# Performance work log

Measured on AMD Instinct MI355X. Metric: run time of the kernel, lower is better.

The kernel has to match this reference:

```python
import jax, jax.numpy as jnp
import numpy as np
import math

B, S, E, H = 2, 4096, 1024, 1024

def setup_inputs() -> dict:
    key = jax.random.key(0)
    ks = jax.random.split(key, 7)
    X = jax.random.normal(ks[0], (B, S, E), dtype=jnp.float32)
    attention_mask = jnp.ones((B, S, S), dtype=jnp.int32)
    sc = 1.0 / math.sqrt(E)
    Wq = jax.random.normal(ks[1], (H, E), dtype=jnp.float32) * sc
    Wk = jax.random.normal(ks[2], (H, E), dtype=jnp.float32) * sc
    Wv = jax.random.normal(ks[3], (H, E), dtype=jnp.float32) * sc
    bq = jnp.zeros((H,), dtype=jnp.float32)
    bk = jnp.zeros((H,), dtype=jnp.float32)
    bv = jnp.zeros((H,), dtype=jnp.float32)
    return {"X": X, "attention_mask": attention_mask,
            "Wq": Wq, "bq": bq, "Wk": Wk, "bk": bk, "Wv": Wv, "bv": bv}

def reference(X, attention_mask, Wq, bq, Wk, bk, Wv, bv):
    # Linear layers: y = x @ W^T + b (torch convention W is [out, in])
    Q = jnp.einsum('bse,he->bsh', X, Wq) + bq
    K = jnp.einsum('bse,he->bsh', X, Wk) + bk
    V = jnp.einsum('bse,he->bsh', X, Wv) + bv
    scale = 1.0 / math.sqrt(H)
    scores = jnp.einsum('bqh,bkh->bqk', Q, K) * scale  # [B,S,S]
    scores = jnp.where(attention_mask == 0, -jnp.inf, scores)
    # dropout (eval mode -> identity) would be applied here, BEFORE softmax
    weights = jax.nn.softmax(scores, axis=-1)
    out = jnp.einsum('bqk,bkh->bqh', weights, V)  # [B,S,H]
    return out
```

## Files before the change

### kernel.cpp

```cpp
#include <hip/hip_runtime.h>
#include <stdint.h>


typedef __bf16 bf16;
typedef __attribute__((ext_vector_type(4))) __bf16 bf16x4;
typedef __attribute__((ext_vector_type(8))) __bf16 bf16x8;
typedef __attribute__((ext_vector_type(4))) float f32x4;

__device__ __forceinline__ void g2l16(const void* g, void* l) {
  __builtin_amdgcn_global_load_lds(
      (const __attribute__((address_space(1))) uint32_t*)g,
      (__attribute__((address_space(3))) uint32_t*)l, 16, 0, 0);
}

template <int N> __device__ __forceinline__ void waitvm() {
  static_assert(N == 0 || N == 3 || N == 4 || N == 6 || N == 8, "vmcnt");
  if constexpr (N == 0) asm volatile("s_waitcnt vmcnt(0)" ::: "memory");
  else if constexpr (N == 3) asm volatile("s_waitcnt vmcnt(3)" ::: "memory");
  else if constexpr (N == 4) asm volatile("s_waitcnt vmcnt(4)" ::: "memory");
  else if constexpr (N == 6) asm volatile("s_waitcnt vmcnt(6)" ::: "memory");
  else asm volatile("s_waitcnt vmcnt(8)" ::: "memory");
}
template <int V> struct IC { static constexpr int value = V; };

__global__ __launch_bounds__(256) void cvt_f32_bf16(
    const float* __restrict__ src, bf16* __restrict__ dst, int n) {
  const int i = (blockIdx.x * 256 + threadIdx.x) * 8;
  if (i >= n) return;
  f32x4 a = *(const f32x4*)(src + i);
  f32x4 b = *(const f32x4*)(src + i + 4);
  bf16x8 o;
#pragma unroll
  for (int e = 0; e < 4; ++e) { o[e] = (bf16)a[e]; o[4 + e] = (bf16)b[e]; }
  *(bf16x8*)(dst + i) = o;
}

__global__ __launch_bounds__(256) void cvt_w3(
    const float* __restrict__ Wq, const float* __restrict__ Wk,
    const float* __restrict__ Wv, bf16* __restrict__ dst) {
  const int i = (blockIdx.x * 256 + threadIdx.x) * 8;
  const int seg = i >> 20;
  const int off = i & 1048575;
  const float* src = (seg == 0) ? Wq : (seg == 1) ? Wk : Wv;
  f32x4 a = *(const f32x4*)(src + off);
  f32x4 b = *(const f32x4*)(src + off + 4);
  bf16x8 o;
#pragma unroll
  for (int e = 0; e < 4; ++e) { o[e] = (bf16)a[e]; o[4 + e] = (bf16)b[e]; }
  *(bf16x8*)(dst + i) = o;
}

template <int BM, int BN, int WM, int WN, int NT>
__device__ __forceinline__ void kloop(
    const bf16* __restrict__ Ag, const bf16* __restrict__ Bg, const int K,
    bf16* lds, f32x4 (&acc)[BM / WM / 16][BN / WN / 16]) {
  constexpr int L = (BM + BN) / 128;
  constexpr int MR = BM / WM / 16, NR = BN / WN / 16;
  const int tid = threadIdx.x;
  const int lane = tid & 63, wave = tid >> 6;
  const int l15 = lane & 15, quad = lane >> 4;
  const int wrow = (wave / WN) * (BM / WM);
  const int wcol = (wave % WN) * (BN / WN);
  const int srow = tid >> 2;
  const int scol = (tid & 3) * 8;

  auto stage = [&](int t) {
    bf16* la = lds + (t & 3) * ((BM + BN) * 32);
    bf16* lb = la + BM * 32;
    const bf16* ga = Ag + (size_t)srow * K + t * 32 + scol;
    const bf16* gb = Bg + (size_t)srow * K + t * 32 + scol;
#pragma unroll
    for (int r = 0; r < BM / 128; ++r)
      g2l16(ga + (size_t)(r * 128) * K, la + (srow + r * 128) * 32 + scol);
#pragma unroll
    for (int r = 0; r < BN / 128; ++r)
      g2l16(gb + (size_t)(r * 128) * K, lb + (srow + r * 128) * 32 + scol);
  };

  stage(0);
  stage(1);
  stage(2);

  auto body = [&](int t, auto vm, bool do_stage) {
    waitvm<decltype(vm)::value>();
    __builtin_amdgcn_s_barrier();
    if (do_stage) stage(t + 3);
    const bf16* la = lds + (t & 3) * ((BM + BN) * 32);
    const bf16* lb = la + BM * 32;
    bf16x8 af[MR], bq[NR];
#pragma unroll
    for (int i = 0; i < MR; ++i)
      af[i] = *(const bf16x8*)&la[(wrow + i * 16 + l15) * 32 + quad * 8];
#pragma unroll
    for (int j = 0; j < NR; ++j)
      bq[j] = *(const bf16x8*)&lb[(wcol + j * 16 + l15) * 32 + quad * 8];
    asm volatile("s_waitcnt lgkmcnt(0)" ::: "memory");
    __builtin_amdgcn_s_setprio(1);
#pragma unroll
    for (int i = 0; i < MR; ++i)
#pragma unroll
      for (int j = 0; j < NR; ++j)
        acc[i][j] = __builtin_amdgcn_mfma_f32_16x16x32_bf16(
            af[i], bq[j], acc[i][j], 0, 0, 0);
    __builtin_amdgcn_s_setprio(0);
  };

  for (int t = 0; t < NT - 2; ++t) body(t, IC<2 * L>{}, t + 3 < NT);
  body(NT - 2, IC<L>{}, false);
  body(NT - 1, IC<0>{}, false);
}

__global__ __launch_bounds__(512, 2) void gemm_qkv(
    const bf16* __restrict__ Xb, const bf16* __restrict__ Wb3,
    const float* __restrict__ bq, const float* __restrict__ bk,
    const float* __restrict__ bv, bf16* __restrict__ QK,
    bf16* __restrict__ Vt) {
  __shared__ __align__(16) bf16 lds[4 * 384 * 32];
  const int which = blockIdx.y >> 3;
  const int n0 = (blockIdx.y & 7) * 128;
  const int m0 = blockIdx.x * 256;
  const bf16* Ag = Xb + (size_t)m0 * 1024;
  const bf16* Bg = Wb3 + (size_t)which * 1048576 + (size_t)n0 * 1024;
  const float* bias = (which == 0) ? bq : ((which == 1) ? bk : bv);

  f32x4 acc[4][4];
#pragma unroll
  for (int i = 0; i < 4; ++i)
#pragma unroll
    for (int j = 0; j < 4; ++j) acc[i][j] = f32x4{0.f, 0.f, 0.f, 0.f};

  kloop<256, 128, 4, 2, 32>(Ag, Bg, 1024, lds, acc);

  const int lane = threadIdx.x & 63, wave = threadIdx.x >> 6;
  const int l15 = lane & 15, quad = lane >> 4;
  const int wrow = (wave >> 1) * 64, wcol = (wave & 1) * 64;

  if (which < 2) {
    bf16* C = QK + (size_t)which * (size_t)(8192 * 1024);
#pragma unroll
    for (int i = 0; i < 4; ++i) {
      const int r = m0 + wrow + i * 16 + quad * 4;
#pragma unroll
      for (int j = 0; j < 4; ++j) {
        const int c = n0 + wcol + j * 16 + l15;
        const float bvv = bias[c];
        f32x4 v = acc[i][j];
#pragma unroll
        for (int reg = 0; reg < 4; ++reg)
          C[(size_t)(r + reg) * 1024 + c] = (bf16)(v[reg] + bvv);
      }
    }
  } else {
#pragma unroll
    for (int i = 0; i < 4; ++i) {
      const int r = m0 + wrow + i * 16 + quad * 4;
      const int b = r >> 12, s = r & 4095;
#pragma unroll
      for (int j = 0; j < 4; ++j) {
        const int c = n0 + wcol + j * 16 + l15;
        const float bvv = bias[c];
        f32x4 v = acc[i][j];
        bf16x4 o;
#pragma unroll
        for (int reg = 0; reg < 4; ++reg) o[reg] = (bf16)(v[reg] + bvv);
        *(bf16x4*)&Vt[((size_t)(b * 1024 + c)) * 4096 + s] = o;
      }
    }
  }
}

__global__ __launch_bounds__(512, 2) void gemm_scores(
    const bf16* __restrict__ Q, const bf16* __restrict__ Kb,
    const int* __restrict__ mask, bf16* __restrict__ P,
    float* __restrict__ row_sum) {
  __shared__ __align__(16) bf16 lds[4 * 512 * 32];
  const int m0 = blockIdx.x * 256;
  const int n0 = blockIdx.y * 256;
  const int batch = m0 >> 12;
  const bf16* Ag = Q + (size_t)m0 * 1024;
  const bf16* Bg = Kb + (size_t)batch * (size_t)(4096 * 1024) +
                   (size_t)n0 * 1024;

  f32x4 acc[8][4];
#pragma unroll
  for (int i = 0; i < 8; ++i)
#pragma unroll
    for (int j = 0; j < 4; ++j) acc[i][j] = f32x4{0.f, 0.f, 0.f, 0.f};

  kloop<256, 256, 2, 4, 32>(Ag, Bg, 1024, lds, acc);

  const int lane = threadIdx.x & 63, wave = threadIdx.x >> 6;
  const int l15 = lane & 15, quad = lane >> 4;
  const int wrow = (wave >> 2) * 128, wcol = (wave & 3) * 64;

#pragma unroll
  for (int i = 0; i < 8; ++i) {
    const int r = m0 + wrow + i * 16 + quad * 4;
    f32x4 rsum = f32x4{0.f, 0.f, 0.f, 0.f};
#pragma unroll
    for (int j = 0; j < 4; ++j) {
      const int c = n0 + wcol + j * 16 + l15;
      f32x4 v = acc[i][j];
#pragma unroll
      for (int reg = 0; reg < 4; ++reg) {
        float e = __expf(v[reg] * 0.03125f);
        if (mask[(size_t)(r + reg) * 4096 + c] == 0) e = 0.f;
        P[(size_t)(r + reg) * 4096 + c] = (bf16)e;
        rsum[reg] += e;
      }
    }
#pragma unroll
    for (int off = 1; off < 16; off <<= 1) {
#pragma unroll
      for (int reg = 0; reg < 4; ++reg)
        rsum[reg] += __shfl_xor(rsum[reg], off);
    }
    if (l15 == 0) {
#pragma unroll
      for (int reg = 0; reg < 4; ++reg)
        atomicAdd(&row_sum[r + reg], rsum[reg]);
    }
  }
}

__global__ __launch_bounds__(512, 2) void gemm_pv(
    const bf16* __restrict__ Pm, const bf16* __restrict__ Vt,
    const float* __restrict__ row_sum, float* __restrict__ C) {
  __shared__ __align__(16) bf16 lds[4 * 384 * 32];
  const int m0 = blockIdx.x * 256;
  const int n0 = blockIdx.y * 128;
  const int batch = m0 >> 12;
  const bf16* Ag = Pm + (size_t)m0 * 4096;
  const bf16* Bg = Vt + ((size_t)batch * 1024 + n0) * 4096;

  f32x4 acc[4][4];
#pragma unroll
  for (int i = 0; i < 4; ++i)
#pragma unroll
    for (int j = 0; j < 4; ++j) acc[i][j] = f32x4{0.f, 0.f, 0.f, 0.f};

  kloop<256, 128, 4, 2, 128>(Ag, Bg, 4096, lds, acc);

  const int lane = threadIdx.x & 63, wave = threadIdx.x >> 6;
  const int l15 = lane & 15, quad = lane >> 4;
  const int wrow = (wave >> 1) * 64, wcol = (wave & 1) * 64;

#pragma unroll
  for (int i = 0; i < 4; ++i) {
    const int r = m0 + wrow + i * 16 + quad * 4;
    const f32x4 rs = *(const f32x4*)&row_sum[r];
    f32x4 inv;
#pragma unroll
    for (int reg = 0; reg < 4; ++reg) inv[reg] = 1.0f / rs[reg];
#pragma unroll
    for (int j = 0; j < 4; ++j) {
      const int c = n0 + wcol + j * 16 + l15;
      f32x4 v = acc[i][j];
#pragma unroll
      for (int reg = 0; reg < 4; ++reg)
        C[(size_t)(r + reg) * 1024 + c] = v[reg] * inv[reg];
    }
  }
}

extern "C" void kernel_launch(void* const* d_in, const int* in_sizes, int n_in,
                              void* d_out, int out_size, void* d_ws,
                              size_t ws_size, hipStream_t stream) {
  const float* X   = (const float*)d_in[0];
  const int* mask  = (const int*)d_in[1];
  const float* Wq  = (const float*)d_in[2];
  const float* bq  = (const float*)d_in[3];
  const float* Wk  = (const float*)d_in[4];
  const float* bk  = (const float*)d_in[5];
  const float* Wv  = (const float*)d_in[6];
  const float* bv  = (const float*)d_in[7];
  float* out = (float*)d_out;

  const size_t QKV_ELEMS = (size_t)8192 * 1024;
  bf16* Q    = (bf16*)d_ws;
  bf16* Kb   = Q + QKV_ELEMS;
  bf16* X_bf = Kb + QKV_ELEMS;
  bf16* Vt   = X_bf + QKV_ELEMS;
  bf16* Sc   = Vt + QKV_ELEMS;
  bf16* W_bf = Sc;
  float* row_sum = (float*)X_bf;

  cvt_f32_bf16<<<dim3(4096), dim3(256), 0, stream>>>(X, X_bf, 8388608);
  cvt_w3<<<dim3(1536), dim3(256), 0, stream>>>(Wq, Wk, Wv, W_bf);
  gemm_qkv<<<dim3(32, 24), dim3(512), 0, stream>>>(X_bf, W_bf, bq, bk, bv, Q,
                                                   Vt);
  hipMemsetAsync(row_sum, 0, 8192 * sizeof(float), stream);
  gemm_scores<<<dim3(32, 16), dim3(512), 0, stream>>>(Q, Kb, mask, Sc,
                                                      row_sum);
  gemm_pv<<<dim3(32, 8), dim3(512), 0, stream>>>(Sc, Vt, row_sum, out);
}
```

Measured before the change: 442.2 us.

## Rewrite GEMM main loops with BK=64, swizzled LDS and phased double-buffered staging

Replaces the generic 4-stage BK=32 k-loop with two specialized kernels, kloop256 and kloop128. Each uses a 64-wide K tile with XOR-swizzled LDS layout to avoid bank conflicts and double buffering. Global-to-LDS loads are split into quarter-tile chunks that are interleaved with MFMA phases, gated by runtime vmcnt waits and extra barriers. The goal is to overlap memory and compute at a finer grain and halve the loop trip count, at the cost of more barriers per tile and intricate hand-sequenced staging that could race if any index is off.

```diff
diff --git a/kernel.cpp b/kernel.cpp
--- a/kernel.cpp
+++ b/kernel.cpp
@@ -13,15 +13,13 @@
       (__attribute__((address_space(3))) uint32_t*)l, 16, 0, 0);
 }
 
-template <int N> __device__ __forceinline__ void waitvm() {
-  static_assert(N == 0 || N == 3 || N == 4 || N == 6 || N == 8, "vmcnt");
-  if constexpr (N == 0) asm volatile("s_waitcnt vmcnt(0)" ::: "memory");
-  else if constexpr (N == 3) asm volatile("s_waitcnt vmcnt(3)" ::: "memory");
-  else if constexpr (N == 4) asm volatile("s_waitcnt vmcnt(4)" ::: "memory");
-  else if constexpr (N == 6) asm volatile("s_waitcnt vmcnt(6)" ::: "memory");
-  else asm volatile("s_waitcnt vmcnt(8)" ::: "memory");
-}
 template <int V> struct IC { static constexpr int value = V; };
+
+__device__ __forceinline__ void waitvm_rt(int vm) {
+  if (vm == 6) asm volatile("s_waitcnt vmcnt(6)" ::: "memory");
+  else if (vm == 4) asm volatile("s_waitcnt vmcnt(4)" ::: "memory");
+  else if (vm == 0) asm volatile("s_waitcnt vmcnt(0)" ::: "memory");
+}
 
 __global__ __launch_bounds__(256) void cvt_f32_bf16(
     const float* __restrict__ src, bf16* __restrict__ dst, int n) {
@@ -50,64 +48,183 @@
   *(bf16x8*)(dst + i) = o;
 }
 
-template <int BM, int BN, int WM, int WN, int NT>
-__device__ __forceinline__ void kloop(
-    const bf16* __restrict__ Ag, const bf16* __restrict__ Bg, const int K,
-    bf16* lds, f32x4 (&acc)[BM / WM / 16][BN / WN / 16]) {
-  constexpr int L = (BM + BN) / 128;
-  constexpr int MR = BM / WM / 16, NR = BN / WN / 16;
+template <int NT>
+__device__ __forceinline__ void kloop256(
+    const bf16* __restrict__ Ag, const bf16* __restrict__ Bg, const int KA,
+    const int KB, bf16* lds, f32x4 (&acc)[8][4]) {
   const int tid = threadIdx.x;
   const int lane = tid & 63, wave = tid >> 6;
   const int l15 = lane & 15, quad = lane >> 4;
-  const int wrow = (wave / WN) * (BM / WM);
-  const int wcol = (wave % WN) * (BN / WN);
-  const int srow = tid >> 2;
-  const int scol = (tid & 3) * 8;
-
-  auto stage = [&](int t) {
-    bf16* la = lds + (t & 3) * ((BM + BN) * 32);
-    bf16* lb = la + BM * 32;
-    const bf16* ga = Ag + (size_t)srow * K + t * 32 + scol;
-    const bf16* gb = Bg + (size_t)srow * K + t * 32 + scol;
-#pragma unroll
-    for (int r = 0; r < BM / 128; ++r)
-      g2l16(ga + (size_t)(r * 128) * K, la + (srow + r * 128) * 32 + scol);
-#pragma unroll
-    for (int r = 0; r < BN / 128; ++r)
-      g2l16(gb + (size_t)(r * 128) * K, lb + (srow + r * 128) * 32 + scol);
+  const int wrow = (wave >> 2) * 128;
+  const int wcol = (wave & 3) * 64;
+  const int srow = tid >> 3;
+  const int scol = ((tid & 7) ^ (srow & 7)) * 8;
+  const int swz = l15 & 7;
+
+  auto stg = [&](int t, int h) {
+    bf16* base = lds + (t & 1) * 32768;
+    if (h == 0) {
+      const bf16* g = Bg + (size_t)srow * KB + t * 64 + scol;
+      g2l16(g, base + 16384 + tid * 8);
+      g2l16(g + (size_t)64 * KB, base + 16384 + tid * 8 + 4096);
+    } else if (h == 1) {
+      const bf16* g = Bg + (size_t)(128 + srow) * KB + t * 64 + scol;
+      g2l16(g, base + 24576 + tid * 8);
+      g2l16(g + (size_t)64 * KB, base + 24576 + tid * 8 + 4096);
+    } else if (h == 2) {
+      const bf16* g = Ag + (size_t)srow * KA + t * 64 + scol;
+      g2l16(g, base + tid * 8);
+      g2l16(g + (size_t)128 * KA, base + tid * 8 + 8192);
+    } else {
+      const bf16* g = Ag + (size_t)(64 + srow) * KA + t * 64 + scol;
+      g2l16(g, base + 4096 + tid * 8);
+      g2l16(g + (size_t)128 * KA, base + 4096 + tid * 8 + 8192);
+    }
   };
 
-  stage(0);
-  stage(1);
-  stage(2);
-
-  auto body = [&](int t, auto vm, bool do_stage) {
-    waitvm<decltype(vm)::value>();
+  bf16x8 bq[2][4];
+  auto phase = [&](int t, auto qc, int st, int sh, bool ds, int vm) {
+    constexpr int q = decltype(qc)::value;
+    bf16* base = lds + (t & 1) * 32768;
+    bf16x8 af[2][2];
+#pragma unroll
+    for (int i = 0; i < 2; ++i)
+#pragma unroll
+      for (int ks = 0; ks < 2; ++ks)
+        af[i][ks] = *(const bf16x8*)&base[
+            (wrow + (2 * q + i) * 16 + l15) * 64 + ((ks * 4 + quad) ^ swz) * 8];
+    if constexpr (q == 0) {
+#pragma unroll
+      for (int j = 0; j < 4; ++j)
+#pragma unroll
+        for (int ks = 0; ks < 2; ++ks)
+          bq[ks][j] = *(const bf16x8*)&base[16384 +
+              (wcol + j * 16 + l15) * 64 + ((ks * 4 + quad) ^ swz) * 8];
+    }
+    if (ds) stg(st, sh);
     __builtin_amdgcn_s_barrier();
-    if (do_stage) stage(t + 3);
-    const bf16* la = lds + (t & 3) * ((BM + BN) * 32);
-    const bf16* lb = la + BM * 32;
-    bf16x8 af[MR], bq[NR];
-#pragma unroll
-    for (int i = 0; i < MR; ++i)
-      af[i] = *(const bf16x8*)&la[(wrow + i * 16 + l15) * 32 + quad * 8];
-#pragma unroll
-    for (int j = 0; j < NR; ++j)
-      bq[j] = *(const bf16x8*)&lb[(wcol + j * 16 + l15) * 32 + quad * 8];
     asm volatile("s_waitcnt lgkmcnt(0)" ::: "memory");
+    __builtin_amdgcn_sched_barrier(0);
     __builtin_amdgcn_s_setprio(1);
 #pragma unroll
-    for (int i = 0; i < MR; ++i)
-#pragma unroll
-      for (int j = 0; j < NR; ++j)
-        acc[i][j] = __builtin_amdgcn_mfma_f32_16x16x32_bf16(
-            af[i], bq[j], acc[i][j], 0, 0, 0);
+    for (int ks = 0; ks < 2; ++ks)
+#pragma unroll
+      for (int i = 0; i < 2; ++i)
+#pragma unroll
+        for (int j = 0; j < 4; ++j)
+          acc[2 * q + i][j] = __builtin_amdgcn_mfma_f32_16x16x32_bf16(
+              af[i][ks], bq[ks][j], acc[2 * q + i][j], 0, 0, 0);
     __builtin_amdgcn_s_setprio(0);
+    waitvm_rt(vm);
+    __builtin_amdgcn_s_barrier();
   };
 
-  for (int t = 0; t < NT - 2; ++t) body(t, IC<2 * L>{}, t + 3 < NT);
-  body(NT - 2, IC<L>{}, false);
-  body(NT - 1, IC<0>{}, false);
+  stg(0, 0); stg(0, 1); stg(0, 2); stg(0, 3);
+  stg(1, 0); stg(1, 1); stg(1, 2);
+  asm volatile("s_waitcnt vmcnt(6)" ::: "memory");
+  __builtin_amdgcn_s_barrier();
+
+  constexpr int NI = NT / 2;
+#pragma unroll 1
+  for (int u = 0; u < NI; ++u) {
+    const int t0 = 2 * u, t1 = t0 + 1;
+    const bool nl = (u + 1 < NI);
+    phase(t0, IC<0>{}, t1, 3, true, -1);
+    phase(t0, IC<1>{}, t0 + 2, 0, nl, -1);
+    phase(t0, IC<2>{}, t0 + 2, 1, nl, -1);
+    phase(t0, IC<3>{}, t0 + 2, 2, nl, nl ? 6 : 0);
+    phase(t1, IC<0>{}, t0 + 2, 3, nl, -1);
+    phase(t1, IC<1>{}, t0 + 3, 0, nl, -1);
+    phase(t1, IC<2>{}, t0 + 3, 1, nl, -1);
+    phase(t1, IC<3>{}, t0 + 3, 2, nl, nl ? 6 : -1);
+  }
+}
+
+template <int NT>
+__device__ __forceinline__ void kloop128(
+    const bf16* __restrict__ Ag, const bf16* __restrict__ Bg, const int KA,
+    const int KB, bf16* lds, f32x4 (&acc)[4][4]) {
+  const int tid = threadIdx.x;
+  const int lane = tid & 63, wave = tid >> 6;
+  const int l15 = lane & 15, quad = lane >> 4;
+  const int wrow = (wave >> 1) * 64;
+  const int wcol = (wave & 1) * 64;
+  const int srow = tid >> 3;
+  const int scol = ((tid & 7) ^ (srow & 7)) * 8;
+  const int swz = l15 & 7;
+  const int s5 = srow >> 5;
+  const int r31 = srow & 31;
+
+  auto stg = [&](int t, int h) {
+    bf16* base = lds + (t & 1) * 24576;
+    if (h == 0) {
+      const bf16* g = Bg + (size_t)srow * KB + t * 64 + scol;
+      g2l16(g, base + 16384 + tid * 8);
+      g2l16(g + (size_t)64 * KB, base + 16384 + tid * 8 + 4096);
+    } else {
+      const int r0 = s5 * 64 + ((h == 2) ? 32 : 0) + r31;
+      const bf16* g = Ag + (size_t)r0 * KA + t * 64 + scol;
+      bf16* d = base + ((h == 2) ? 2048 : 0) + s5 * 4096 + r31 * 64 +
+                (tid & 7) * 8;
+      g2l16(g, d);
+      g2l16(g + (size_t)128 * KA, d + 8192);
+    }
+  };
+
+  bf16x8 bq[2][4];
+  auto phase = [&](int t, auto mhc, int st1, int sh1, int st2, int sh2,
+                   bool ds, int vm) {
+    constexpr int mh = decltype(mhc)::value;
+    bf16* base = lds + (t & 1) * 24576;
+    bf16x8 af[2][2];
+#pragma unroll
+    for (int i = 0; i < 2; ++i)
+#pragma unroll
+      for (int ks = 0; ks < 2; ++ks)
+        af[i][ks] = *(const bf16x8*)&base[
+            (wrow + (2 * mh + i) * 16 + l15) * 64 +
+            ((ks * 4 + quad) ^ swz) * 8];
+    if constexpr (mh == 0) {
+#pragma unroll
+      for (int j = 0; j < 4; ++j)
+#pragma unroll
+        for (int ks = 0; ks < 2; ++ks)
+          bq[ks][j] = *(const bf16x8*)&base[16384 +
+              (wcol + j * 16 + l15) * 64 + ((ks * 4 + quad) ^ swz) * 8];
+    }
+    if (ds) { stg(st1, sh1); if (sh2 >= 0) stg(st2, sh2); }
+    __builtin_amdgcn_s_barrier();
+    asm volatile("s_waitcnt lgkmcnt(0)" ::: "memory");
+    __builtin_amdgcn_sched_barrier(0);
+    __builtin_amdgcn_s_setprio(1);
+#pragma unroll
+    for (int ks = 0; ks < 2; ++ks)
+#pragma unroll
+      for (int i = 0; i < 2; ++i)
+#pragma unroll
+        for (int j = 0; j < 4; ++j)
+          acc[2 * mh + i][j] = __builtin_amdgcn_mfma_f32_16x16x32_bf16(
+              af[i][ks], bq[ks][j], acc[2 * mh + i][j], 0, 0, 0);
+    __builtin_amdgcn_s_setprio(0);
+    waitvm_rt(vm);
+    __builtin_amdgcn_s_barrier();
+  };
+
+  stg(0, 0); stg(0, 1); stg(0, 2);
+  stg(1, 0); stg(1, 1);
+  asm volatile("s_waitcnt vmcnt(4)" ::: "memory");
+  __builtin_amdgcn_s_barrier();
+
+  constexpr int NI = NT / 2;
+#pragma unroll 1
+  for (int u = 0; u < NI; ++u) {
+    const int t0 = 2 * u, t1 = t0 + 1;
+    const bool nl = (u + 1 < NI);
+    phase(t0, IC<0>{}, t1, 2, -1, -1, true, -1);
+    phase(t0, IC<1>{}, t0 + 2, 0, t0 + 2, 1, nl, nl ? 4 : 0);
+    phase(t1, IC<0>{}, t0 + 2, 2, -1, -1, nl, -1);
+    phase(t1, IC<1>{}, t0 + 3, 0, t0 + 3, 1, nl, nl ? 4 : -1);
+  }
 }
 
 __global__ __launch_bounds__(512, 2) void gemm_qkv(
@@ -115,7 +232,7 @@
     const float* __restrict__ bq, const float* __restrict__ bk,
     const float* __restrict__ bv, bf16* __restrict__ QK,
     bf16* __restrict__ Vt) {
-  __shared__ __align__(16) bf16 lds[4 * 384 * 32];
+  __shared__ __align__(16) bf16 lds[2 * 24576];
   const int which = blockIdx.y >> 3;
   const int n0 = (blockIdx.y & 7) * 128;
   const int m0 = blockIdx.x * 256;
@@ -129,7 +246,7 @@
 #pragma unroll
     for (int j = 0; j < 4; ++j) acc[i][j] = f32x4{0.f, 0.f, 0.f, 0.f};
 
-  kloop<256, 128, 4, 2, 32>(Ag, Bg, 1024, lds, acc);
+  kloop128<16>(Ag, Bg, 1024, 1024, lds, acc);
 
   const int lane = threadIdx.x & 63, wave = threadIdx.x >> 6;
   const int l15 = lane & 15, quad = lane >> 4;
@@ -173,7 +290,7 @@
     const bf16* __restrict__ Q, const bf16* __restrict__ Kb,
     const int* __restrict__ mask, bf16* __restrict__ P,
     float* __restrict__ row_sum) {
-  __shared__ __align__(16) bf16 lds[4 * 512 * 32];
+  __shared__ __align__(16) bf16 lds[2 * 32768];
   const int m0 = blockIdx.x * 256;
   const int n0 = blockIdx.y * 256;
   const int batch = m0 >> 12;
@@ -187,7 +304,7 @@
 #pragma unroll
     for (int j = 0; j < 4; ++j) acc[i][j] = f32x4{0.f, 0.f, 0.f, 0.f};
 
-  kloop<256, 256, 2, 4, 32>(Ag, Bg, 1024, lds, acc);
+  kloop256<16>(Ag, Bg, 1024, 1024, lds, acc);
 
   const int lane = threadIdx.x & 63, wave = threadIdx.x >> 6;
   const int l15 = lane & 15, quad = lane >> 4;
@@ -226,7 +343,7 @@
 __global__ __launch_bounds__(512, 2) void gemm_pv(
     const bf16* __restrict__ Pm, const bf16* __restrict__ Vt,
     const float* __restrict__ row_sum, float* __restrict__ C) {
-  __shared__ __align__(16) bf16 lds[4 * 384 * 32];
+  __shared__ __align__(16) bf16 lds[2 * 24576];
   const int m0 = blockIdx.x * 256;
   const int n0 = blockIdx.y * 128;
   const int batch = m0 >> 12;
@@ -239,7 +356,7 @@
 #pragma unroll
     for (int j = 0; j < 4; ++j) acc[i][j] = f32x4{0.f, 0.f, 0.f, 0.f};
 
-  kloop<256, 128, 4, 2, 128>(Ag, Bg, 4096, lds, acc);
+  kloop128<64>(Ag, Bg, 4096, 4096, lds, acc);
 
   const int lane = threadIdx.x & 63, wave = threadIdx.x >> 6;
   const int l15 = lane & 15, quad = lane >> 4;
```

New measurement: 434.3 us. Within noise of the previous version (-1.8%).
